# Optimization experiments

Measured on AMD Instinct MI355X. Metric: run time of the kernel, lower is better.

## Reference

```python
import jax, jax.numpy as jnp
import numpy as np

B, D, T = 16, 512, 2048
H = 2
HD = D // H

def setup_inputs() -> dict:
    key = jax.random.key(0)
    k1, k2, k3, k4 = jax.random.split(key, 4)
    s_in = 1.0 / np.sqrt(D)   # torch default-like uniform init for weight_matrix
    s_t = 1.0 / np.sqrt(T)    # nn.Linear default init bound
    xs = jax.random.normal(k1, (B, D, T), dtype=jnp.float32)
    W_KQ = jax.random.uniform(k2, (D, D), jnp.float32, -s_in, s_in)
    W_PV = jax.random.uniform(k3, (D, D), jnp.float32, -s_in, s_in)
    W_out = jax.random.uniform(k4, (T, T), jnp.float32, -s_t, s_t)
    return {"xs": xs, "W_KQ": W_KQ, "W_PV": W_PV, "W_out": W_out}

def reference(xs, W_KQ, W_PV, W_out):
    b, d, t = xs.shape
    xs_skip = xs[:, :, :-1]                                   # [B, D, T-1]
    # xskq = xs_skip^T @ W_KQ  -> [B, T-1, D]
    xskq = jnp.einsum('bds,dj->bsj', xs_skip, W_KQ)
    # split heads: [B, H, T-1, HD]
    xskq_split = xskq.reshape(b, t - 1, H, HD).transpose(0, 2, 1, 3)
    # xs reshaped to heads along feature dim: [B, H, HD, T]
    xs_r = xs.reshape(b, H, HD, t)
    attn_arg = jnp.matmul(xskq_split, xs_r)                   # [B, H, T-1, T], rho=1
    # NON-STANDARD: softmax over the head axis (size 2)
    sm = jax.nn.softmax(attn_arg, axis=1)
    # W_PV @ xs_skip -> [B, D, T-1], split into heads [B, H, HD, T-1]
    wpvx = jnp.einsum('id,bds->bis', W_PV, xs_skip).reshape(b, H, HD, t - 1)
    f_attn = jnp.matmul(wpvx, sm).reshape(b, d, t)            # [B, D, T]
    # output = Linear(T, T, bias=None) then take last token:
    # out[b, i] = sum_t f_attn[b, i, t] * W_out[T-1, t]
    out = jnp.einsum('bdt,t->bd', f_attn, W_out[-1])
    return out
```

## Files before the change

kernel.cpp:

```cpp
#include <hip/hip_runtime.h>
#include <hip/hip_bf16.h>

#define NB 16
#define ND 512
#define NT 2048
#define TM1 2047
#define NHD 256

typedef __attribute__((ext_vector_type(8))) short bf16x8;
typedef __attribute__((ext_vector_type(4))) float f32x4;
typedef unsigned short ushort_t;
typedef unsigned int uint_t;

#define G0_OFF    0ull
#define R0_OFF    32768ull
#define SX_OFF    40960ull
#define WSUM_OFF  49152ull
#define WKQT_OFF  49408ull
#define CHUNK_OFF 180480ull
#define BATCH_US  (2048ull * 512ull)
#define BATCH_FLOATS (2ull * 524288ull)

__device__ __forceinline__ ushort_t f2bf(float x) {
    union { float f; uint_t u; } v; v.f = x;
    uint_t r = v.u + 0x7FFFu + ((v.u >> 16) & 1u);
    return (ushort_t)(r >> 16);
}
__device__ __forceinline__ float bf2f(uint_t u) {
    union { uint_t u; float f; } v; v.u = u << 16;
    return v.f;
}

__device__ __forceinline__ void async_copy16(const ushort_t* g, ushort_t* l) {
    __builtin_amdgcn_global_load_lds(
        (const __attribute__((address_space(1))) void*)g,
        (__attribute__((address_space(3))) void*)l, 16, 0, 0);
}

#define FENCE() asm volatile("" ::: "memory")
#define BARRIER() do { FENCE(); __builtin_amdgcn_s_barrier(); FENCE(); } while (0)
#define WAITVM4() asm volatile("s_waitcnt vmcnt(4)" ::: "memory")
#define WAITVM0() asm volatile("s_waitcnt vmcnt(0)" ::: "memory")

__global__ __launch_bounds__(256) void k_cvt_xst(const float* __restrict__ xs,
                                                 ushort_t* __restrict__ xst, int b0,
                                                 const float* __restrict__ wkq,
                                                 ushort_t* __restrict__ wkqT,
                                                 const float* __restrict__ wlast,
                                                 float* __restrict__ wsum,
                                                 float* __restrict__ zbase) {
    __shared__ float tile[64][257];
    const int t0 = blockIdx.x * 256, d0 = blockIdx.y * 64;
    const int cc = blockIdx.z;
    const float* xb = xs + (size_t)(b0 + cc) * ND * NT;
    ushort_t* xo = xst + (size_t)cc * BATCH_US;
    const int wave = threadIdx.x >> 6, lane = threadIdx.x & 63;
    #pragma unroll
    for (int i = 0; i < 16; ++i) {
        const int row = wave * 16 + i;
        *(float4*)&tile[row][lane * 4] =
            *(const float4*)&xb[(size_t)(d0 + row) * NT + t0 + lane * 4];
    }
    __syncthreads();
    const int c8 = (threadIdx.x & 7) * 8;
    #pragma unroll
    for (int i = 0; i < 8; ++i) {
        const int t = i * 32 + (threadIdx.x >> 3);
        uint_t w[4];
        #pragma unroll
        for (int p = 0; p < 4; ++p)
            w[p] = (uint_t)f2bf(tile[c8 + 2 * p][t]) |
                   ((uint_t)f2bf(tile[c8 + 2 * p + 1][t]) << 16);
        *(uint4*)&xo[(size_t)(t0 + t) * ND + d0 + c8] = *(uint4*)w;
    }
    if (cc == 0 && b0 == 0) {
        __shared__ float ptile[32][33];
        const int bid = blockIdx.y * 8 + blockIdx.x;
        const int c = threadIdx.x & 31, r = threadIdx.x >> 5;
        #pragma unroll 1
        for (int q = 0; q < 4; ++q) {
            const int job = bid * 4 + q;
            const int j0 = (job & 15) * 32, dd0 = (job >> 4) * 32;
            __syncthreads();
            #pragma unroll
            for (int i = 0; i < 4; ++i)
                ptile[r + i * 8][c] = wkq[(size_t)(dd0 + r + i * 8) * ND + j0 + c];
            __syncthreads();
            #pragma unroll
            for (int i = 0; i < 4; ++i)
                wkqT[(size_t)(j0 + r + i * 8) * ND + dd0 + c] = f2bf(ptile[c][r + i * 8]);
        }
        #pragma unroll
        for (int k = 0; k < 3; ++k)
            zbase[bid * 768 + k * 256 + threadIdx.x] = 0.f;
        if (bid == 0) {
            __shared__ float red[256];
            float s = 0.f;
            for (int t = threadIdx.x; t < NT; t += 256) s += wlast[t];
            red[threadIdx.x] = s;
            __syncthreads();
            for (int off = 128; off > 0; off >>= 1) {
                if (threadIdx.x < off) red[threadIdx.x] += red[threadIdx.x + off];
                __syncthreads();
            }
            if (threadIdx.x == 0) *wsum = red[0];
        }
    }
}

__device__ __forceinline__ void ld_frag4(bf16x8 (&dst)[4][2], const ushort_t* buf,
                                         int rbase, int l15, int quad, int swz) {
    #pragma unroll
    for (int i = 0; i < 4; ++i)
        #pragma unroll
        for (int kc = 0; kc < 2; ++kc)
            dst[i][kc] = *(const bf16x8*)&buf[(rbase + i * 16 + l15) * 64 + (((kc * 4 + quad) ^ swz) << 3)];
}
__device__ __forceinline__ void ld_frag2(bf16x8 (&dst)[2][2], const ushort_t* buf,
                                         int rbase, int l15, int quad, int swz) {
    #pragma unroll
    for (int i = 0; i < 2; ++i)
        #pragma unroll
        for (int kc = 0; kc < 2; ++kc)
            dst[i][kc] = *(const bf16x8*)&buf[(rbase + i * 16 + l15) * 64 + (((kc * 4 + quad) ^ swz) << 3)];
}
__device__ __forceinline__ void mfma8(f32x4 (&acc)[8][4], const bf16x8 (&a)[4][2],
                                      const bf16x8 (&bb)[2][2], int mbase, int nbase) {
    __builtin_amdgcn_s_setprio(1);
    #pragma unroll
    for (int kc = 0; kc < 2; ++kc)
        #pragma unroll
        for (int mi = 0; mi < 4; ++mi)
            #pragma unroll
            for (int nj = 0; nj < 2; ++nj)
                acc[mbase + mi][nbase + nj] = __builtin_amdgcn_mfma_f32_16x16x32_bf16(
                    a[mi][kc], bb[nj][kc], acc[mbase + mi][nbase + nj], 0, 0, 0);
    __builtin_amdgcn_s_setprio(0);
}

__device__ __forceinline__ void gemm8ph(const ushort_t* __restrict__ Ag,
                                        const ushort_t* __restrict__ Bg,
                                        ushort_t* __restrict__ smA0, ushort_t* __restrict__ smA1,
                                        ushort_t* __restrict__ smB0, ushort_t* __restrict__ smB1,
                                        f32x4 (&acc)[8][4]) {
    const int tid = threadIdx.x;
    const int wave = tid >> 6, lane = tid & 63;
    const int l15 = lane & 15, quad = lane >> 4;
    const int wm = wave >> 2;
    const int swz = l15 & 7;
    const int lrow = lane >> 3;
    const size_t lsrc = (size_t)lrow * ND + (size_t)(((lane & 7) ^ lrow) << 3);
    ushort_t* smA[2] = {smA0, smA1};
    ushort_t* smB[2] = {smB0, smB1};

#define STAGE(gb_, buf_, kt_, h_) do {                                        \
        const ushort_t* g_ = (gb_) + (size_t)((h_) * 128 + wave * 8) * ND +   \
                             (kt_) * 64 + lsrc;                               \
        ushort_t* l_ = (buf_) + (h_) * 8192 + wave * 512;                     \
        async_copy16(g_, l_);                                                 \
        async_copy16(g_ + (size_t)64 * ND, l_ + 4096);                        \
    } while (0)

    bf16x8 a[4][2], br[2][2][2];

    STAGE(Bg, smB[0], 0, 0); STAGE(Bg, smB[0], 0, 1);
    STAGE(Ag, smA[0], 0, 0); STAGE(Ag, smA[0], 0, 1);
    STAGE(Bg, smB[1], 1, 0); STAGE(Bg, smB[1], 1, 1);
    WAITVM4();
    BARRIER();

    #pragma unroll
    for (int j = 0; j < 4; ++j) {
        const int kO = 2 * j + 1;
        ld_frag4(a, smA[0], wm * 128, l15, quad, swz);
        ld_frag2(br[0], smB[0], (wave & 3) * 64, l15, quad, swz);
        STAGE(Ag, smA[1], kO, 0);
        BARRIER();
        mfma8(acc, a, br[0], 0, 0);
        BARRIER();
        ld_frag2(br[1], smB[0], (wave & 3) * 64 + 32, l15, quad, swz);
        STAGE(Ag, smA[1], kO, 1);
        BARRIER();
        mfma8(acc, a, br[1], 0, 2);
        BARRIER();
        ld_frag4(a, smA[0], wm * 128 + 64, l15, quad, swz);
        if (j < 3) STAGE(Bg, smB[0], 2 * j + 2, 0);
        BARRIER();
        mfma8(acc, a, br[0], 4, 0);
        BARRIER();
        if (j < 3) STAGE(Bg, smB[0], 2 * j + 2, 1);
        BARRIER();
        mfma8(acc, a, br[1], 4, 2);
        if (j < 3) { WAITVM4(); } else { WAITVM0(); }
        BARRIER();
        ld_frag4(a, smA[1], wm * 128, l15, quad, swz);
        ld_frag2(br[0], smB[1], (wave & 3) * 64, l15, quad, swz);
        if (j < 3) STAGE(Ag, smA[0], 2 * j + 2, 0);
        BARRIER();
        mfma8(acc, a, br[0], 0, 0);
        BARRIER();
        ld_frag2(br[1], smB[1], (wave & 3) * 64 + 32, l15, quad, swz);
        if (j < 3) STAGE(Ag, smA[0], 2 * j + 2, 1);
        BARRIER();
        mfma8(acc, a, br[1], 0, 2);
        BARRIER();
        ld_frag4(a, smA[1], wm * 128 + 64, l15, quad, swz);
        if (j < 3) STAGE(Bg, smB[1], kO + 2, 0);
        BARRIER();
        mfma8(acc, a, br[0], 4, 0);
        BARRIER();
        if (j < 3) STAGE(Bg, smB[1], kO + 2, 1);
        BARRIER();
        mfma8(acc, a, br[1], 4, 2);
        if (j < 3) WAITVM4();
        BARRIER();
    }
#undef STAGE
}

__global__ __launch_bounds__(512, 2) void k_qd(const ushort_t* __restrict__ xst,
                                               const ushort_t* __restrict__ wkqT,
                                               ushort_t* __restrict__ qdb) {
    __shared__ __align__(16) ushort_t smA[2][16384];
    __shared__ __align__(16) ushort_t smB[2][16384];
    const int lin = blockIdx.x + gridDim.x * (blockIdx.y + gridDim.y * blockIdx.z);
    const int nwg8 = (gridDim.x * gridDim.y * gridDim.z) >> 3;
    const int logical = (lin & 7) * nwg8 + (lin >> 3);
    const int jt = logical & 1;
    const int st = (logical >> 1) & 7;
    const int cc = logical >> 4;
    const int j0 = jt * 256, s0 = st * 256;

    const ushort_t* Ag = xst + (size_t)cc * BATCH_US + (size_t)s0 * ND;
    const ushort_t* Bg = wkqT + (size_t)j0 * ND;
    ushort_t* qo = qdb + (size_t)cc * BATCH_US;

    f32x4 acc[8][4];
    #pragma unroll
    for (int mi = 0; mi < 8; ++mi)
        #pragma unroll
        for (int nj = 0; nj < 4; ++nj) acc[mi][nj] = (f32x4){0.f, 0.f, 0.f, 0.f};

    gemm8ph(Ag, Bg, smA[0], smA[1], smB[0], smB[1], acc);

    const int tid = threadIdx.x;
    const int wave = tid >> 6, lane = tid & 63;
    const int l15 = lane & 15, quad = lane >> 4;
    const int wm = wave >> 2, wn = wave & 3;
    const float sgn = (j0 == 0) ? 1.f : -1.f;
    #pragma unroll
    for (int mi = 0; mi < 8; ++mi) {
        const int srow = s0 + wm * 128 + mi * 16 + quad * 4;
        #pragma unroll
        for (int nj = 0; nj < 4; ++nj) {
            const int jcol = j0 + wn * 64 + nj * 16 + l15;
            #pragma unroll
            for (int r = 0; r < 4; ++r)
                qo[(size_t)(srow + r) * ND + jcol] = f2bf(sgn * acc[mi][nj][r]);
        }
    }
}

__global__ __launch_bounds__(256, 4) void k_attn(const ushort_t* __restrict__ qdb,
                                                 const ushort_t* __restrict__ xst,
                                                 const float* __restrict__ wlast,
                                                 float* __restrict__ g0, int b0) {
    __shared__ __align__(16) ushort_t smA[8192];
    __shared__ __align__(16) ushort_t smB[8192];
    __shared__ float lds_g[128];
    const int lin = blockIdx.x + gridDim.x * (blockIdx.y + gridDim.y * blockIdx.z);
    const int nwg8 = (gridDim.x * gridDim.y * gridDim.z) >> 3;
    const int logical = (lin & 7) * nwg8 + (lin >> 3);
    const int st = logical & 15;
    const int tq = (logical >> 4) & 3;
    const int cc = logical >> 6;
    const int s0 = st * 128;
    const int b = b0 + cc;

    const int tid = threadIdx.x;
    const int wave = tid >> 6, lane = tid & 63;
    const int l15 = lane & 15, quad = lane >> 4;
    const int wm = wave >> 1, wn = wave & 1;
    const int swz = l15 & 7;
    const int lrow = lane >> 3;
    const size_t lsrc = (size_t)lrow * ND + (size_t)(((lane & 7) ^ lrow) << 3);
    const ushort_t* Ag = qdb + (size_t)cc * BATCH_US + (size_t)s0 * ND;
    const ushort_t* Bg = xst + (size_t)cc * BATCH_US + (size_t)(tq * 512) * ND;

#define STAGEA(kt_) do {                                                      \
        const size_t ko_ = (size_t)(kt_) * 64;                                \
        _Pragma("unroll")                                                     \
        for (int n_ = 0; n_ < 4; ++n_) {                                      \
            const int rb_ = wave * 32 + n_ * 8;                               \
            async_copy16(Ag + (size_t)rb_ * ND + ko_ + lsrc, smA + rb_ * 64); \
        }                                                                     \
    } while (0)
#define STAGEB(kt_, tt_) do {                                                 \
        const size_t ko_ = (size_t)(kt_) * 64;                                \
        const size_t ro_ = (size_t)(tt_) * 128;                               \
        _Pragma("unroll")                                                     \
        for (int n_ = 0; n_ < 4; ++n_) {                                      \
            const int rb_ = wave * 32 + n_ * 8;                               \
            async_copy16(Bg + (ro_ + rb_) * ND + ko_ + lsrc, smB + rb_ * 64); \
        }                                                                     \
    } while (0)
#define COMPUTE() do {                                                        \
        _Pragma("unroll")                                                     \
        for (int kc = 0; kc < 2; ++kc) {                                      \
            bf16x8 af_[4], bf_[4];                                            \
            _Pragma("unroll")                                                 \
            for (int mi = 0; mi < 4; ++mi)                                    \
                af_[mi] = *(const bf16x8*)&smA[(wm * 64 + mi * 16 + l15) * 64 \
                          + (((kc * 4 + quad) ^ swz) << 3)];                  \
            _Pragma("unroll")                                                 \
            for (int nj = 0; nj < 4; ++nj)                                    \
                bf_[nj] = *(const bf16x8*)&smB[(wn * 64 + nj * 16 + l15) * 64 \
                          + (((kc * 4 + quad) ^ swz) << 3)];                  \
            __builtin_amdgcn_s_setprio(1);                                    \
            _Pragma("unroll")                                                 \
            for (int mi = 0; mi < 4; ++mi)                                    \
                _Pragma("unroll")                                             \
                for (int nj = 0; nj < 4; ++nj)                                \
                    acc[mi][nj] = __builtin_amdgcn_mfma_f32_16x16x32_bf16(    \
                        af_[mi], bf_[nj], acc[mi][nj], 0, 0, 0);              \
            __builtin_amdgcn_s_setprio(0);                                    \
        }                                                                     \
    } while (0)

    f32x4 acc[4][4];
    #pragma unroll
    for (int mi = 0; mi < 4; ++mi)
        #pragma unroll
        for (int nj = 0; nj < 4; ++nj) acc[mi][nj] = (f32x4){0.f, 0.f, 0.f, 0.f};
    if (tid < 128) lds_g[tid] = 0.f;

    #pragma unroll 1
    for (int it = 0; it < 32; ++it) {
        const int kt = it & 7, tt = it >> 3;
        STAGEA(kt);
        STAGEB(kt, tt);
        WAITVM0();
        BARRIER();
        COMPUTE();
        if (kt == 7) {
            const int tb = tq * 512 + tt * 128;
            float wt[4];
            #pragma unroll
            for (int nj = 0; nj < 4; ++nj) wt[nj] = wlast[tb + wn * 64 + nj * 16 + l15];
            #pragma unroll
            for (int mi = 0; mi < 4; ++mi)
                #pragma unroll
                for (int r = 0; r < 4; ++r) {
                    float v = 0.f;
                    #pragma unroll
                    for (int nj = 0; nj < 4; ++nj) {
                        const float e = __expf(-acc[mi][nj][r]);
                        v = fmaf(__builtin_amdgcn_rcpf(1.f + e), wt[nj], v);
                    }
                    v += __shfl_xor(v, 1);
                    v += __shfl_xor(v, 2);
                    v += __shfl_xor(v, 4);
                    v += __shfl_xor(v, 8);
                    if (l15 == 0) atomicAdd(&lds_g[wm * 64 + mi * 16 + quad * 4 + r], v);
                }
            #pragma unroll
            for (int mi = 0; mi < 4; ++mi)
                #pragma unroll
                for (int nj = 0; nj < 4; ++nj) acc[mi][nj] = (f32x4){0.f, 0.f, 0.f, 0.f};
        }
        BARRIER();
    }
#undef STAGEA
#undef STAGEB
#undef COMPUTE

    __syncthreads();
    if (tid < 128) {
        const int srow = s0 + tid;
        if (srow < TM1) atomicAdd(&g0[b * TM1 + srow], lds_g[tid]);
    }
}

__global__ __launch_bounds__(256) void k_r(const ushort_t* __restrict__ xst,
                                           const float* __restrict__ g0,
                                           float* __restrict__ r0acc,
                                           float* __restrict__ sxacc, int b0) {
    const int sc = blockIdx.x;
    const int cc = blockIdx.y;
    const int b = b0 + cc;
    const ushort_t* xa = xst + (size_t)cc * BATCH_US;
    const float* g = g0 + b * TM1;
    const int d2 = threadIdx.x;
    float a00 = 0.f, a01 = 0.f, a10 = 0.f, a11 = 0.f;
    const int send = (sc == 31) ? 63 : 64;
    for (int si = 0; si < send; ++si) {
        const int s = sc * 64 + si;
        const float gv = g[s];
        const uint_t pk = *(const uint_t*)&xa[(size_t)s * ND + d2 * 2];
        const float x0 = bf2f(pk & 0xFFFFu);
        const float x1 = bf2f(pk >> 16);
        a00 = fmaf(x0, gv, a00); a01 = fmaf(x1, gv, a01);
        a10 += x0; a11 += x1;
    }
    atomicAdd(&r0acc[b * ND + d2 * 2], a00);
    atomicAdd(&r0acc[b * ND + d2 * 2 + 1], a01);
    atomicAdd(&sxacc[b * ND + d2 * 2], a10);
    atomicAdd(&sxacc[b * ND + d2 * 2 + 1], a11);
}

__global__ __launch_bounds__(256) void k_out(const float* __restrict__ wpv,
                                             const float* __restrict__ r0acc,
                                             const float* __restrict__ sxacc,
                                             const float* __restrict__ wsum,
                                             float* __restrict__ out) {
    const int b = blockIdx.x;
    const int i0 = blockIdx.y * 256;
    __shared__ float rs[1024];
    const float wsv = *wsum;
    for (int i = threadIdx.x; i < ND; i += 256) {
        const float r0 = r0acc[b * ND + i];
        const float sx = sxacc[b * ND + i];
        rs[i] = r0;
        rs[ND + i] = fmaf(wsv, sx, -r0);
    }
    __syncthreads();
    const int i = i0 + threadIdx.x;
    const float* wrow = wpv + (size_t)i * ND;
    const float* rh = rs + (i >> 8) * ND;
    float acc = 0.f;
    for (int dd = 0; dd < ND; dd += 4) {
        const float4 wv = *(const float4*)(wrow + dd);
        acc += wv.x * rh[dd] + wv.y * rh[dd + 1] + wv.z * rh[dd + 2] + wv.w * rh[dd + 3];
    }
    out[b * ND + i] = acc;
}

extern "C" void kernel_launch(void* const* d_in, const int* in_sizes, int n_in,
                              void* d_out, int out_size, void* d_ws, size_t ws_size,
                              hipStream_t stream) {
    (void)in_sizes; (void)n_in; (void)out_size;
    const float* xs   = (const float*)d_in[0];
    const float* wkq  = (const float*)d_in[1];
    const float* wpv  = (const float*)d_in[2];
    const float* wout = (const float*)d_in[3];
    const float* wlast = wout + (size_t)(NT - 1) * NT;

    float* ws    = (float*)d_ws;
    float* g0    = ws + G0_OFF;
    float* r0acc = ws + R0_OFF;
    float* sxacc = ws + SX_OFF;
    float* wsum  = ws + WSUM_OFF;
    ushort_t* wkqT = (ushort_t*)(ws + WKQT_OFF);

    const size_t ws_floats = ws_size / 4;
    size_t avail = (ws_floats > CHUNK_OFF) ? (ws_floats - CHUNK_OFF) : 0;
    int C = (int)(avail / BATCH_FLOATS);
    if (C > NB) C = NB;
    if (C < 1) C = 1;
    ushort_t* qdb = (ushort_t*)(ws + CHUNK_OFF);
    ushort_t* xst = (ushort_t*)(ws + CHUNK_OFF + (size_t)C * 524288ull);

    for (int b0 = 0; b0 < NB; b0 += C) {
        const int cb = (NB - b0 < C) ? (NB - b0) : C;
        k_cvt_xst<<<dim3(8, 8, cb), 256, 0, stream>>>(xs, xst, b0,
                                                      wkq, wkqT, wlast, wsum, ws);
        k_qd     <<<dim3(2, 8, cb),  512, 0, stream>>>(xst, wkqT, qdb);
        k_attn   <<<dim3(16, 4, cb), 256, 0, stream>>>(qdb, xst, wlast, g0, b0);
        k_r      <<<dim3(32, cb),    256, 0, stream>>>(xst, g0, r0acc, sxacc, b0);
    }
    k_out<<<dim3(NB, 2), 256, 0, stream>>>(wpv, r0acc, sxacc, wsum, (float*)d_out);
}
```

Measured before the change: 261.0 us.

## Fuse k_r reduction into k_attn epilogue and column sums into conversion

Removes the separate k_r kernel. Each attention block now multiplies its 128-row slice of the gate vector, held in LDS, with the matching bf16 xs rows and atomically adds the result into r0acc. The column sums sx are computed inside the transpose/convert kernel, and the per-iteration shuffle reduction is deferred to a single one after the loop. Zeroing moves to a hipMemsetAsync. This drops one launch and the g0 round-trip through global memory, at the cost of more global atomics, since the four tq blocks per slice each redo the xs read, and a heavier attention epilogue.

```diff
diff --git a/kernel.cpp b/kernel.cpp
--- a/kernel.cpp
+++ b/kernel.cpp
@@ -48,13 +48,15 @@
                                                  ushort_t* __restrict__ wkqT,
                                                  const float* __restrict__ wlast,
                                                  float* __restrict__ wsum,
-                                                 float* __restrict__ zbase) {
+                                                 float* __restrict__ sxacc) {
     __shared__ float tile[64][257];
+    __shared__ float sxl[64];
     const int t0 = blockIdx.x * 256, d0 = blockIdx.y * 64;
     const int cc = blockIdx.z;
     const float* xb = xs + (size_t)(b0 + cc) * ND * NT;
     ushort_t* xo = xst + (size_t)cc * BATCH_US;
     const int wave = threadIdx.x >> 6, lane = threadIdx.x & 63;
+    if (threadIdx.x < 64) sxl[threadIdx.x] = 0.f;
     #pragma unroll
     for (int i = 0; i < 16; ++i) {
         const int row = wave * 16 + i;
@@ -63,6 +65,7 @@
     }
     __syncthreads();
     const int c8 = (threadIdx.x & 7) * 8;
+    float sxp[8] = {0.f, 0.f, 0.f, 0.f, 0.f, 0.f, 0.f, 0.f};
     #pragma unroll
     for (int i = 0; i < 8; ++i) {
         const int t = i * 32 + (threadIdx.x >> 3);
@@ -72,7 +75,16 @@
             w[p] = (uint_t)f2bf(tile[c8 + 2 * p][t]) |
                    ((uint_t)f2bf(tile[c8 + 2 * p + 1][t]) << 16);
         *(uint4*)&xo[(size_t)(t0 + t) * ND + d0 + c8] = *(uint4*)w;
-    }
+        if (t0 + t != 2047) {
+            #pragma unroll
+            for (int p = 0; p < 8; ++p) sxp[p] += tile[c8 + p][t];
+        }
+    }
+    #pragma unroll
+    for (int p = 0; p < 8; ++p) atomicAdd(&sxl[c8 + p], sxp[p]);
+    __syncthreads();
+    if (threadIdx.x < 64)
+        atomicAdd(&sxacc[(size_t)(b0 + cc) * ND + d0 + threadIdx.x], sxl[threadIdx.x]);
     if (cc == 0 && b0 == 0) {
         __shared__ float ptile[32][33];
         const int bid = blockIdx.y * 8 + blockIdx.x;
@@ -90,9 +102,6 @@
             for (int i = 0; i < 4; ++i)
                 wkqT[(size_t)(j0 + r + i * 8) * ND + dd0 + c] = f2bf(ptile[c][r + i * 8]);
         }
-        #pragma unroll
-        for (int k = 0; k < 3; ++k)
-            zbase[bid * 768 + k * 256 + threadIdx.x] = 0.f;
         if (bid == 0) {
             __shared__ float red[256];
             float s = 0.f;
@@ -264,7 +273,7 @@
 __global__ __launch_bounds__(256, 4) void k_attn(const ushort_t* __restrict__ qdb,
                                                  const ushort_t* __restrict__ xst,
                                                  const float* __restrict__ wlast,
-                                                 float* __restrict__ g0, int b0) {
+                                                 float* __restrict__ r0acc, int b0) {
     __shared__ __align__(16) ushort_t smA[8192];
     __shared__ __align__(16) ushort_t smB[8192];
     __shared__ float lds_g[128];
@@ -328,10 +337,11 @@
     } while (0)
 
     f32x4 acc[4][4];
+    float gp[4][4];
     #pragma unroll
     for (int mi = 0; mi < 4; ++mi)
         #pragma unroll
-        for (int nj = 0; nj < 4; ++nj) acc[mi][nj] = (f32x4){0.f, 0.f, 0.f, 0.f};
+        for (int nj = 0; nj < 4; ++nj) { acc[mi][nj] = (f32x4){0.f, 0.f, 0.f, 0.f}; gp[mi][nj] = 0.f; }
     if (tid < 128) lds_g[tid] = 0.f;
 
     #pragma unroll 1
@@ -351,17 +361,11 @@
             for (int mi = 0; mi < 4; ++mi)
                 #pragma unroll
                 for (int r = 0; r < 4; ++r) {
-                    float v = 0.f;
                     #pragma unroll
                     for (int nj = 0; nj < 4; ++nj) {
                         const float e = __expf(-acc[mi][nj][r]);
-                        v = fmaf(__builtin_amdgcn_rcpf(1.f + e), wt[nj], v);
+                        gp[mi][r] = fmaf(__builtin_amdgcn_rcpf(1.f + e), wt[nj], gp[mi][r]);
                     }
-                    v += __shfl_xor(v, 1);
-                    v += __shfl_xor(v, 2);
-                    v += __shfl_xor(v, 4);
-                    v += __shfl_xor(v, 8);
-                    if (l15 == 0) atomicAdd(&lds_g[wm * 64 + mi * 16 + quad * 4 + r], v);
                 }
             #pragma unroll
             for (int mi = 0; mi < 4; ++mi)
@@ -374,38 +378,31 @@
 #undef STAGEB
 #undef COMPUTE
 
+    #pragma unroll
+    for (int mi = 0; mi < 4; ++mi)
+        #pragma unroll
+        for (int r = 0; r < 4; ++r) {
+            float v = gp[mi][r];
+            v += __shfl_xor(v, 1);
+            v += __shfl_xor(v, 2);
+            v += __shfl_xor(v, 4);
+            v += __shfl_xor(v, 8);
+            if (l15 == 0) atomicAdd(&lds_g[wm * 64 + mi * 16 + quad * 4 + r], v);
+        }
     __syncthreads();
-    if (tid < 128) {
-        const int srow = s0 + tid;
-        if (srow < TM1) atomicAdd(&g0[b * TM1 + srow], lds_g[tid]);
-    }
-}
-
-__global__ __launch_bounds__(256) void k_r(const ushort_t* __restrict__ xst,
-                                           const float* __restrict__ g0,
-                                           float* __restrict__ r0acc,
-                                           float* __restrict__ sxacc, int b0) {
-    const int sc = blockIdx.x;
-    const int cc = blockIdx.y;
-    const int b = b0 + cc;
-    const ushort_t* xa = xst + (size_t)cc * BATCH_US;
-    const float* g = g0 + b * TM1;
-    const int d2 = threadIdx.x;
-    float a00 = 0.f, a01 = 0.f, a10 = 0.f, a11 = 0.f;
-    const int send = (sc == 31) ? 63 : 64;
-    for (int si = 0; si < send; ++si) {
-        const int s = sc * 64 + si;
-        const float gv = g[s];
-        const uint_t pk = *(const uint_t*)&xa[(size_t)s * ND + d2 * 2];
-        const float x0 = bf2f(pk & 0xFFFFu);
-        const float x1 = bf2f(pk >> 16);
-        a00 = fmaf(x0, gv, a00); a01 = fmaf(x1, gv, a01);
-        a10 += x0; a11 += x1;
-    }
-    atomicAdd(&r0acc[b * ND + d2 * 2], a00);
-    atomicAdd(&r0acc[b * ND + d2 * 2 + 1], a01);
-    atomicAdd(&sxacc[b * ND + d2 * 2], a10);
-    atomicAdd(&sxacc[b * ND + d2 * 2 + 1], a11);
+    {
+        const ushort_t* xrow = xst + (size_t)cc * BATCH_US + (size_t)s0 * ND;
+        const int send = (st == 15) ? 127 : 128;
+        float a0 = 0.f, a1 = 0.f;
+        for (int si = 0; si < send; ++si) {
+            const float gv = lds_g[si];
+            const uint_t pk = *(const uint_t*)&xrow[(size_t)si * ND + tid * 2];
+            a0 = fmaf(bf2f(pk & 0xFFFFu), gv, a0);
+            a1 = fmaf(bf2f(pk >> 16), gv, a1);
+        }
+        atomicAdd(&r0acc[(size_t)b * ND + tid * 2], a0);
+        atomicAdd(&r0acc[(size_t)b * ND + tid * 2 + 1], a1);
+    }
 }
 
 __global__ __launch_bounds__(256) void k_out(const float* __restrict__ wpv,
@@ -446,7 +443,6 @@
     const float* wlast = wout + (size_t)(NT - 1) * NT;
 
     float* ws    = (float*)d_ws;
-    float* g0    = ws + G0_OFF;
     float* r0acc = ws + R0_OFF;
     float* sxacc = ws + SX_OFF;
     float* wsum  = ws + WSUM_OFF;
@@ -460,13 +456,14 @@
     ushort_t* qdb = (ushort_t*)(ws + CHUNK_OFF);
     ushort_t* xst = (ushort_t*)(ws + CHUNK_OFF + (size_t)C * 524288ull);
 
+    hipMemsetAsync(r0acc, 0, 16384 * sizeof(float), stream);
+
     for (int b0 = 0; b0 < NB; b0 += C) {
         const int cb = (NB - b0 < C) ? (NB - b0) : C;
         k_cvt_xst<<<dim3(8, 8, cb), 256, 0, stream>>>(xs, xst, b0,
-                                                      wkq, wkqT, wlast, wsum, ws);
+                                                      wkq, wkqT, wlast, wsum, sxacc);
         k_qd     <<<dim3(2, 8, cb),  512, 0, stream>>>(xst, wkqT, qdb);
-        k_attn   <<<dim3(16, 4, cb), 256, 0, stream>>>(qdb, xst, wlast, g0, b0);
-        k_r      <<<dim3(32, cb),    256, 0, stream>>>(xst, g0, r0acc, sxacc, b0);
+        k_attn   <<<dim3(16, 4, cb), 256, 0, stream>>>(qdb, xst, wlast, r0acc, b0);
     }
     k_out<<<dim3(NB, 2), 256, 0, stream>>>(wpv, r0acc, sxacc, wsum, (float*)d_out);
 }
```

Result: no change. 263.0 us (+0.7%).
